# Kernel optimization log

Hardware: AMD Instinct MI355X
Metric: run time of the kernel (lower is better)

Reference implementation:

```python
import jax, jax.numpy as jnp
import numpy as np

D_MODEL = 1024
N_HEADS = 16
D_HEAD = D_MODEL // N_HEADS
SEQ = 2048
BATCH = 2


def setup_inputs() -> dict:
    key = jax.random.key(0)
    ks = jax.random.split(key, 9)
    s = 1.0 / np.sqrt(D_MODEL)
    inp = {
        "x": jax.random.normal(ks[0], (BATCH, SEQ, D_MODEL), dtype=jnp.float32),
        "Wq": jax.random.uniform(ks[1], (D_MODEL, D_MODEL), jnp.float32, -s, s),
        "bq": jax.random.uniform(ks[2], (D_MODEL,), jnp.float32, -s, s),
        "Wk": jax.random.uniform(ks[3], (D_MODEL, D_MODEL), jnp.float32, -s, s),
        "bk": jax.random.uniform(ks[4], (D_MODEL,), jnp.float32, -s, s),
        "Wv": jax.random.uniform(ks[5], (D_MODEL, D_MODEL), jnp.float32, -s, s),
        "bv": jax.random.uniform(ks[6], (D_MODEL,), jnp.float32, -s, s),
        "Wo": jax.random.uniform(ks[7], (D_MODEL, D_MODEL), jnp.float32, -s, s),
        "bo": jax.random.uniform(ks[8], (D_MODEL,), jnp.float32, -s, s),
    }
    return inp


def reference(x, Wq, bq, Wk, bk, Wv, bv, Wo, bo):
    B, S, D = x.shape
    H, Dh = N_HEADS, D_HEAD
    # QKV projections (nn.Linear: x @ W.T + b; here W stored as [in, out])
    q = (x @ Wq + bq).reshape(B, S, H, Dh).transpose(0, 2, 1, 3)  # [B,H,S,Dh]
    k = (x @ Wk + bk).reshape(B, S, H, Dh).transpose(0, 2, 1, 3)
    v = (x @ Wv + bv).reshape(B, S, H, Dh).transpose(0, 2, 1, 3)
    scores = jnp.einsum("bhqd,bhkd->bhqk", q, k) / jnp.sqrt(jnp.float32(Dh))
    causal = jnp.tril(jnp.ones((S, S), dtype=bool))  # [S,S]
    scores = jnp.where(causal[None, None], scores, jnp.float32(-jnp.inf))
    attn = jax.nn.softmax(scores, axis=-1)
    # dropout is identity in eval mode
    h = jnp.einsum("bhqk,bhkd->bhqd", attn, v)  # [B,H,S,Dh]
    h = h.transpose(0, 2, 1, 3).reshape(B, S, D)
    return h @ Wo + bo
```

## Files before the change

### kernel.cpp

```cpp
#include <hip/hip_runtime.h>

typedef unsigned short u16;
typedef unsigned int u32;
typedef __attribute__((ext_vector_type(8))) __bf16 bf16x8;
typedef __attribute__((ext_vector_type(4))) float f32x4;
typedef __attribute__((ext_vector_type(4))) unsigned short u16x4;

#define SEQ 2048
#define DM 1024
#define NH 16
#define DH 64

__device__ __forceinline__ float fexp2(float x) {
  return __builtin_amdgcn_exp2f(x);
}

__device__ __forceinline__ unsigned short f2bf(float f) {
  unsigned u = __builtin_bit_cast(unsigned, f);
  u += 0x7fffu + ((u >> 16) & 1u);
  return (unsigned short)(u >> 16);
}

__device__ __forceinline__ void gload_lds16(const u16* g, u16* l) {
  __builtin_amdgcn_global_load_lds(
      (const __attribute__((address_space(1))) u16*)g,
      (__attribute__((address_space(3))) u16*)l, 16, 0, 0);
}

__global__ __launch_bounds__(256) void cvt_kernel(const float* __restrict__ in,
                                                  u16* __restrict__ out, int n4) {
  int id = blockIdx.x * 256 + threadIdx.x;
  if (id >= n4) return;
  float4 v = ((const float4*)in)[id];
  u16x4 o = { f2bf(v.x), f2bf(v.y), f2bf(v.z), f2bf(v.w) };
  ((u16x4*)out)[id] = o;
}

__global__ __launch_bounds__(256) void wtrans_kernel(const float* __restrict__ W0,
                                                     const float* __restrict__ W1,
                                                     const float* __restrict__ W2,
                                                     const float* __restrict__ W3,
                                                     u16* __restrict__ WtBase) {
  const float* W = (blockIdx.z == 0) ? W0 : (blockIdx.z == 1) ? W1
                 : (blockIdx.z == 2) ? W2 : W3;
  u16* Wt = WtBase + ((size_t)blockIdx.z << 20);
  __shared__ float tile[32][33];
  int tx = threadIdx.x & 31, ty = threadIdx.x >> 5;
  int k0 = blockIdx.y * 32, n0 = blockIdx.x * 32;
#pragma unroll
  for (int j = 0; j < 32; j += 8)
    tile[ty + j][tx] = W[(size_t)(k0 + ty + j) * DM + n0 + tx];
  __syncthreads();
#pragma unroll
  for (int j = 0; j < 32; j += 8)
    Wt[(size_t)(n0 + ty + j) * DM + k0 + tx] = f2bf(tile[tx][ty + j]);
}

__global__ __launch_bounds__(256) void gemm_kernel(
    const u16* __restrict__ A, const u16* __restrict__ WtBase,
    const float* __restrict__ b0, const float* __restrict__ b1,
    const float* __restrict__ b2,
    void* __restrict__ O0, void* __restrict__ O1, void* __restrict__ O2,
    int modeBase) {
  const int Kd = 1024, Nd = 1024;
  const int mode = modeBase + blockIdx.z;
  const u16* Bt = WtBase + (size_t)blockIdx.z * (1u << 20);
  const float* bias = (blockIdx.z == 0) ? b0 : (blockIdx.z == 1) ? b1 : b2;
  void* Out = (blockIdx.z == 0) ? O0 : (blockIdx.z == 1) ? O1 : O2;

  __shared__ u16 As[2][4096];
  __shared__ u16 Bs[2][4096];
  const int tid = threadIdx.x;
  const int lane = tid & 63, w = tid >> 6;
  const int lrow = lane & 15, u = lane >> 4;
  const int wr = w >> 1, wc = w & 1;
  const int brow = blockIdx.y * 128, bcol = blockIdx.x * 128;

  f32x4 acc[4][4] = {};

  const int srow = tid >> 2;
  const int scol = (tid & 3) * 8;
  const u16* a0 = A + (size_t)(brow + srow) * Kd + scol;
  const u16* a1 = A + (size_t)(brow + 64 + srow) * Kd + scol;
  const u16* bt0 = Bt + (size_t)(bcol + srow) * Kd + scol;
  const u16* bt1 = Bt + (size_t)(bcol + 64 + srow) * Kd + scol;

  auto stage = [&](int kt, int buf) {
    gload_lds16(a0 + kt, As[buf] + w * 512);
    gload_lds16(a1 + kt, As[buf] + 2048 + w * 512);
    gload_lds16(bt0 + kt, Bs[buf] + w * 512);
    gload_lds16(bt1 + kt, Bs[buf] + 2048 + w * 512);
  };

  stage(0, 0);
  __syncthreads();

  for (int it = 0; it < 32; ++it) {
    const int cur = it & 1;
    if (it + 1 < 32) stage((it + 1) * 32, cur ^ 1);
    bf16x8 af[4], bfr[4];
#pragma unroll
    for (int m = 0; m < 4; ++m)
      af[m] = *(const bf16x8*)(As[cur] + (wr * 64 + m * 16 + lrow) * 32 + u * 8);
#pragma unroll
    for (int n = 0; n < 4; ++n)
      bfr[n] = *(const bf16x8*)(Bs[cur] + (wc * 64 + n * 16 + lrow) * 32 + u * 8);
#pragma unroll
    for (int m = 0; m < 4; ++m)
#pragma unroll
      for (int n = 0; n < 4; ++n)
        acc[m][n] = __builtin_amdgcn_mfma_f32_16x16x32_bf16(af[m], bfr[n], acc[m][n], 0, 0, 0);
    __syncthreads();
  }

  const int r0 = brow + wr * 64 + u * 4;
  const int c0 = bcol + wc * 64 + lrow;
#pragma unroll
  for (int m = 0; m < 4; ++m) {
#pragma unroll
    for (int n = 0; n < 4; ++n) {
      const int col = c0 + n * 16;
      const float bv = bias[col];
      if (mode == 3) {
        float* O = (float*)Out;
#pragma unroll
        for (int i = 0; i < 4; ++i) {
          int row = r0 + m * 16 + i;
          O[(size_t)row * Nd + col] = acc[m][n][i] + bv;
        }
      } else if (mode == 2) {
        const int rowb = r0 + m * 16;
        const int b = rowb >> 11, s = rowb & 2047;
        const int h = col >> 6, dh = col & 63;
        u16x4 pk;
#pragma unroll
        for (int i = 0; i < 4; ++i) pk[i] = f2bf(acc[m][n][i] + bv);
        u16* O = (u16*)Out;
        *(u16x4*)(O + ((size_t)((b * NH + h) * DH + dh) * SEQ + s)) = pk;
      } else {
        const float sc = (mode == 0) ? 0.1803368801111204f : 1.0f;
        u16* O = (u16*)Out;
#pragma unroll
        for (int i = 0; i < 4; ++i) {
          int row = r0 + m * 16 + i;
          int b = row >> 11, s = row & 2047;
          int h = col >> 6, dh = col & 63;
          O[((size_t)(b * NH + h) * SEQ + s) * DH + dh] = f2bf((acc[m][n][i] + bv) * sc);
        }
      }
    }
  }
}

__device__ __forceinline__ void process_tile(
    const u16* bufK, const u16* bufV, u16* ps,
    const bf16x8 (&qf)[2], f32x4 (&hacc)[4], float& m_i, float& l_i,
    int lrow, int u, int wq, bool diag) {
  f32x4 s[4] = {};
#pragma unroll
  for (int ks = 0; ks < 2; ++ks) {
    const int c = ks * 64 + u * 16;
#pragma unroll
    for (int g = 0; g < 4; ++g) {
      const int r = g * 16 + lrow;
      const bf16x8 kf = *(const bf16x8*)(bufK + ((r * 128 + (c ^ ((r & 7) << 4))) >> 1));
      s[g] = __builtin_amdgcn_mfma_f32_16x16x32_bf16(kf, qf[ks], s[g], 0, 0, 0);
    }
  }
  if (diag) {
#pragma unroll
    for (int g = 0; g < 4; ++g) {
      const int kb = g * 16 + u * 4;
#pragma unroll
      for (int i = 0; i < 4; ++i)
        if (kb + i > wq) s[g][i] = -1e30f;
    }
  }
  float pg[4];
#pragma unroll
  for (int g = 0; g < 4; ++g)
    pg[g] = fmaxf(fmaxf(s[g][0], s[g][1]), fmaxf(s[g][2], s[g][3]));
  float pmax = fmaxf(fmaxf(pg[0], pg[1]), fmaxf(pg[2], pg[3]));
  pmax = fmaxf(pmax, __shfl_xor(pmax, 16));
  pmax = fmaxf(pmax, __shfl_xor(pmax, 32));
  const float mnew = fmaxf(m_i, pmax);
  const float scl = fexp2(m_i - mnew);
  float rs = 0.f;
#pragma unroll
  for (int g = 0; g < 4; ++g)
#pragma unroll
    for (int i = 0; i < 4; ++i) {
      const float p = fexp2(s[g][i] - mnew);
      s[g][i] = p;
      rs += p;
    }
  rs += __shfl_xor(rs, 16);
  rs += __shfl_xor(rs, 32);
  l_i = l_i * scl + rs;
  m_i = mnew;
#pragma unroll
  for (int g = 0; g < 4; ++g) hacc[g] *= scl;
#pragma unroll
  for (int g = 0; g < 4; ++g)
#pragma unroll
    for (int h = 0; h < 2; ++h) {
      const u32 w32 = (u32)f2bf(s[g][2 * h]) | ((u32)f2bf(s[g][2 * h + 1]) << 16);
      const int cb = (g * 16 + u * 4 + 2 * h) * 2;
      *(u32*)(ps + ((lrow * 128 + (cb ^ ((lrow & 7) << 4))) >> 1)) = w32;
    }
#pragma unroll
  for (int ks = 0; ks < 2; ++ks) {
    const int c = ks * 64 + u * 16;
    const bf16x8 pf = *(const bf16x8*)(ps + ((lrow * 128 + (c ^ ((lrow & 7) << 4))) >> 1));
#pragma unroll
    for (int g = 0; g < 4; ++g) {
      const int r = g * 16 + lrow;
      const bf16x8 vf = *(const bf16x8*)(bufV + ((r * 128 + (c ^ ((r & 7) << 4))) >> 1));
      hacc[g] = __builtin_amdgcn_mfma_f32_16x16x32_bf16(vf, pf, hacc[g], 0, 0, 0);
    }
  }
}

__global__ __launch_bounds__(256, 2) void attn_kernel(const u16* __restrict__ Qb,
                                                      const u16* __restrict__ Kb,
                                                      const u16* __restrict__ Vt,
                                                      u16* __restrict__ Hh) {
  const int px = blockIdx.x, bh = blockIdx.y;
  const int qtA = px, qtB = 31 - px;
  const int tid = threadIdx.x, lane = tid & 63, w = tid >> 6;
  const int lrow = lane & 15, u = lane >> 4;

  const u16* Qp = Qb + (size_t)bh * SEQ * DH;
  const u16* Kp = Kb + (size_t)bh * SEQ * DH;
  const u16* Vp = Vt + (size_t)bh * DH * SEQ;

  __shared__ u16 KV[2][2][4096];
  __shared__ u16 Ps[4][1024];

  const int q0A = qtA * 64 + w * 16, q0B = qtB * 64 + w * 16;
  bf16x8 qfA[2], qfB[2];
#pragma unroll
  for (int ks = 0; ks < 2; ++ks) {
    qfA[ks] = *(const bf16x8*)(Qp + (size_t)(q0A + lrow) * DH + ks * 32 + u * 8);
    qfB[ks] = *(const bf16x8*)(Qp + (size_t)(q0B + lrow) * DH + ks * 32 + u * 8);
  }

  float mA = -1e30f, lA = 0.f, mB = -1e30f, lB = 0.f;
  f32x4 haccA[4], haccB[4];
#pragma unroll
  for (int g = 0; g < 4; ++g) {
    haccA[g] = (f32x4){0.f, 0.f, 0.f, 0.f};
    haccB[g] = (f32x4){0.f, 0.f, 0.f, 0.f};
  }

  auto stage = [&](int kt, int buf) {
#pragma unroll
    for (int i = 0; i < 2; ++i) {
      const int p = i * 4096 + tid * 16;
      const int row = p >> 7;
      const int c16 = ((p >> 4) & 7) ^ (row & 7);
      gload_lds16(Kp + (size_t)(kt * 64 + row) * 64 + c16 * 8, &KV[buf][0][p >> 1]);
      gload_lds16(Vp + (size_t)row * 2048 + (size_t)kt * 64 + c16 * 8, &KV[buf][1][p >> 1]);
    }
  };

  stage(0, 0);
  __syncthreads();

  const int wq = w * 16 + lrow;
  const int nkt = qtB + 1;
  for (int kt = 0; kt < nkt; ++kt) {
    const int cur = kt & 1;
    if (kt + 1 < nkt) stage(kt + 1, cur ^ 1);
    if (kt <= qtA)
      process_tile(KV[cur][0], KV[cur][1], Ps[w], qfA, haccA, mA, lA, lrow, u, wq, kt == qtA);
    process_tile(KV[cur][0], KV[cur][1], Ps[w], qfB, haccB, mB, lB, lrow, u, wq, kt == qtB);
    __syncthreads();
  }

  const int b = bh >> 4, h = bh & 15;
  {
    const float inv = 1.0f / lA;
    u16* dst = Hh + ((size_t)b * SEQ + (q0A + lrow)) * DM + h * DH + u * 4;
#pragma unroll
    for (int g = 0; g < 4; ++g) {
      u16x4 pk = { f2bf(haccA[g][0] * inv), f2bf(haccA[g][1] * inv),
                   f2bf(haccA[g][2] * inv), f2bf(haccA[g][3] * inv) };
      *(u16x4*)(dst + g * 16) = pk;
    }
  }
  {
    const float inv = 1.0f / lB;
    u16* dst = Hh + ((size_t)b * SEQ + (q0B + lrow)) * DM + h * DH + u * 4;
#pragma unroll
    for (int g = 0; g < 4; ++g) {
      u16x4 pk = { f2bf(haccB[g][0] * inv), f2bf(haccB[g][1] * inv),
                   f2bf(haccB[g][2] * inv), f2bf(haccB[g][3] * inv) };
      *(u16x4*)(dst + g * 16) = pk;
    }
  }
}

extern "C" void kernel_launch(void* const* d_in, const int* in_sizes, int n_in,
                              void* d_out, int out_size, void* d_ws, size_t ws_size,
                              hipStream_t stream) {
  const float* x  = (const float*)d_in[0];
  const float* Wq = (const float*)d_in[1];
  const float* bq = (const float*)d_in[2];
  const float* Wk = (const float*)d_in[3];
  const float* bk = (const float*)d_in[4];
  const float* Wv = (const float*)d_in[5];
  const float* bv = (const float*)d_in[6];
  const float* Wo = (const float*)d_in[7];
  const float* bo = (const float*)d_in[8];
  float* out = (float*)d_out;

  char* ws = (char*)d_ws;
  u16* Xb  = (u16*)(ws);
  u16* Wt  = (u16*)(ws + (8u << 20));
  u16* Qb  = (u16*)(ws + (16u << 20));
  u16* Kb  = (u16*)(ws + (24u << 20));
  u16* Vt  = (u16*)(ws + (32u << 20));
  u16* Hh  = (u16*)(ws + (40u << 20));
  (void)in_sizes; (void)n_in; (void)out_size; (void)ws_size;

  cvt_kernel<<<4096, 256, 0, stream>>>(x, Xb, 4096 * 1024 / 4);
  dim3 tg(32, 32, 4);
  wtrans_kernel<<<tg, 256, 0, stream>>>(Wq, Wk, Wv, Wo, Wt);
  dim3 gq(8, 32, 3);
  gemm_kernel<<<gq, 256, 0, stream>>>(Xb, Wt, bq, bk, bv, Qb, Kb, Vt, 0);
  dim3 ga(16, 32);
  attn_kernel<<<ga, 256, 0, stream>>>(Qb, Kb, Vt, Hh);
  dim3 go(8, 32, 1);
  gemm_kernel<<<go, 256, 0, stream>>>(Hh, Wt + (3u << 20), bo, bo, bo, out, out, out, 3);
}
```

Before: 204.3 us.

## Interleave dual-query attention tiles, lazy softmax rescale, packed bf16 cvt, smaller GEMM tiles

The attention loop now loads K and V fragments once per tile and shares them between the two query tiles. It also interleaves their MFMAs and gives each query tile its own P scratch buffer. Softmax rescaling is skipped unless the running max grows by more than 8 (in log2 units), which cuts exp work and accumulator scaling but lets unnormalised values reach up to 2^8. Float-to-bf16 conversion uses the hardware packed-convert instruction, and the GEMMs are templated onto smaller tiles to launch more blocks. The extra fragment registers may raise register pressure.

```diff
diff --git a/kernel.cpp b/kernel.cpp
--- a/kernel.cpp
+++ b/kernel.cpp
@@ -5,6 +5,7 @@
 typedef __attribute__((ext_vector_type(8))) __bf16 bf16x8;
 typedef __attribute__((ext_vector_type(4))) float f32x4;
 typedef __attribute__((ext_vector_type(4))) unsigned short u16x4;
+typedef __attribute__((ext_vector_type(2))) unsigned int u32x2;
 
 #define SEQ 2048
 #define DM 1024
@@ -19,6 +20,12 @@
   unsigned u = __builtin_bit_cast(unsigned, f);
   u += 0x7fffu + ((u >> 16) & 1u);
   return (unsigned short)(u >> 16);
+}
+
+__device__ __forceinline__ u32 cvtpk(float lo, float hi) {
+  u32 r;
+  asm("v_cvt_pk_bf16_f32 %0, %1, %2" : "=v"(r) : "v"(lo), "v"(hi));
+  return r;
 }
 
 __device__ __forceinline__ void gload_lds16(const u16* g, u16* l) {
@@ -56,40 +63,42 @@
     Wt[(size_t)(n0 + ty + j) * DM + k0 + tx] = f2bf(tile[tx][ty + j]);
 }
 
+template <int BM, int BN>
 __global__ __launch_bounds__(256) void gemm_kernel(
     const u16* __restrict__ A, const u16* __restrict__ WtBase,
     const float* __restrict__ b0, const float* __restrict__ b1,
     const float* __restrict__ b2,
     void* __restrict__ O0, void* __restrict__ O1, void* __restrict__ O2,
     int modeBase) {
+  constexpr int MR = BM / 32, NR = BN / 32;
   const int Kd = 1024, Nd = 1024;
   const int mode = modeBase + blockIdx.z;
-  const u16* Bt = WtBase + (size_t)blockIdx.z * (1u << 20);
+  const u16* Bt = WtBase + ((size_t)blockIdx.z << 20);
   const float* bias = (blockIdx.z == 0) ? b0 : (blockIdx.z == 1) ? b1 : b2;
   void* Out = (blockIdx.z == 0) ? O0 : (blockIdx.z == 1) ? O1 : O2;
 
-  __shared__ u16 As[2][4096];
-  __shared__ u16 Bs[2][4096];
+  __shared__ u16 As[2][BM * 32];
+  __shared__ u16 Bs[2][BN * 32];
   const int tid = threadIdx.x;
   const int lane = tid & 63, w = tid >> 6;
   const int lrow = lane & 15, u = lane >> 4;
   const int wr = w >> 1, wc = w & 1;
-  const int brow = blockIdx.y * 128, bcol = blockIdx.x * 128;
-
-  f32x4 acc[4][4] = {};
+  const int brow = blockIdx.y * BM, bcol = blockIdx.x * BN;
+
+  f32x4 acc[MR][NR] = {};
 
   const int srow = tid >> 2;
   const int scol = (tid & 3) * 8;
-  const u16* a0 = A + (size_t)(brow + srow) * Kd + scol;
-  const u16* a1 = A + (size_t)(brow + 64 + srow) * Kd + scol;
-  const u16* bt0 = Bt + (size_t)(bcol + srow) * Kd + scol;
-  const u16* bt1 = Bt + (size_t)(bcol + 64 + srow) * Kd + scol;
+  const u16* aP = A + (size_t)(brow + srow) * Kd + scol;
+  const u16* bP = Bt + (size_t)(bcol + srow) * Kd + scol;
 
   auto stage = [&](int kt, int buf) {
-    gload_lds16(a0 + kt, As[buf] + w * 512);
-    gload_lds16(a1 + kt, As[buf] + 2048 + w * 512);
-    gload_lds16(bt0 + kt, Bs[buf] + w * 512);
-    gload_lds16(bt1 + kt, Bs[buf] + 2048 + w * 512);
+#pragma unroll
+    for (int i = 0; i < BM / 64; ++i)
+      gload_lds16(aP + (size_t)i * 64 * Kd + kt, As[buf] + i * 2048 + w * 512);
+#pragma unroll
+    for (int i = 0; i < BN / 64; ++i)
+      gload_lds16(bP + (size_t)i * 64 * Kd + kt, Bs[buf] + i * 2048 + w * 512);
   };
 
   stage(0, 0);
@@ -98,27 +107,27 @@
   for (int it = 0; it < 32; ++it) {
     const int cur = it & 1;
     if (it + 1 < 32) stage((it + 1) * 32, cur ^ 1);
-    bf16x8 af[4], bfr[4];
-#pragma unroll
-    for (int m = 0; m < 4; ++m)
-      af[m] = *(const bf16x8*)(As[cur] + (wr * 64 + m * 16 + lrow) * 32 + u * 8);
-#pragma unroll
-    for (int n = 0; n < 4; ++n)
-      bfr[n] = *(const bf16x8*)(Bs[cur] + (wc * 64 + n * 16 + lrow) * 32 + u * 8);
-#pragma unroll
-    for (int m = 0; m < 4; ++m)
-#pragma unroll
-      for (int n = 0; n < 4; ++n)
+    bf16x8 af[MR], bfr[NR];
+#pragma unroll
+    for (int m = 0; m < MR; ++m)
+      af[m] = *(const bf16x8*)(As[cur] + (wr * (BM / 2) + m * 16 + lrow) * 32 + u * 8);
+#pragma unroll
+    for (int n = 0; n < NR; ++n)
+      bfr[n] = *(const bf16x8*)(Bs[cur] + (wc * (BN / 2) + n * 16 + lrow) * 32 + u * 8);
+#pragma unroll
+    for (int m = 0; m < MR; ++m)
+#pragma unroll
+      for (int n = 0; n < NR; ++n)
         acc[m][n] = __builtin_amdgcn_mfma_f32_16x16x32_bf16(af[m], bfr[n], acc[m][n], 0, 0, 0);
     __syncthreads();
   }
 
-  const int r0 = brow + wr * 64 + u * 4;
-  const int c0 = bcol + wc * 64 + lrow;
-#pragma unroll
-  for (int m = 0; m < 4; ++m) {
-#pragma unroll
-    for (int n = 0; n < 4; ++n) {
+  const int r0 = brow + wr * (BM / 2) + u * 4;
+  const int c0 = bcol + wc * (BN / 2) + lrow;
+#pragma unroll
+  for (int m = 0; m < MR; ++m) {
+#pragma unroll
+    for (int n = 0; n < NR; ++n) {
       const int col = c0 + n * 16;
       const float bv = bias[col];
       if (mode == 3) {
@@ -152,72 +161,42 @@
   }
 }
 
-__device__ __forceinline__ void process_tile(
-    const u16* bufK, const u16* bufV, u16* ps,
-    const bf16x8 (&qf)[2], f32x4 (&hacc)[4], float& m_i, float& l_i,
-    int lrow, int u, int wq, bool diag) {
-  f32x4 s[4] = {};
-#pragma unroll
-  for (int ks = 0; ks < 2; ++ks) {
-    const int c = ks * 64 + u * 16;
-#pragma unroll
-    for (int g = 0; g < 4; ++g) {
-      const int r = g * 16 + lrow;
-      const bf16x8 kf = *(const bf16x8*)(bufK + ((r * 128 + (c ^ ((r & 7) << 4))) >> 1));
-      s[g] = __builtin_amdgcn_mfma_f32_16x16x32_bf16(kf, qf[ks], s[g], 0, 0, 0);
-    }
-  }
-  if (diag) {
-#pragma unroll
-    for (int g = 0; g < 4; ++g) {
-      const int kb = g * 16 + u * 4;
-#pragma unroll
-      for (int i = 0; i < 4; ++i)
-        if (kb + i > wq) s[g][i] = -1e30f;
-    }
-  }
-  float pg[4];
-#pragma unroll
-  for (int g = 0; g < 4; ++g)
-    pg[g] = fmaxf(fmaxf(s[g][0], s[g][1]), fmaxf(s[g][2], s[g][3]));
-  float pmax = fmaxf(fmaxf(pg[0], pg[1]), fmaxf(pg[2], pg[3]));
+__device__ __forceinline__ void softmax_update(f32x4 (&s)[4], f32x4 (&hacc)[4],
+                                               float& m_i, float& l_i) {
+  float pg0 = fmaxf(fmaxf(s[0][0], s[0][1]), fmaxf(s[0][2], s[0][3]));
+  float pg1 = fmaxf(fmaxf(s[1][0], s[1][1]), fmaxf(s[1][2], s[1][3]));
+  float pg2 = fmaxf(fmaxf(s[2][0], s[2][1]), fmaxf(s[2][2], s[2][3]));
+  float pg3 = fmaxf(fmaxf(s[3][0], s[3][1]), fmaxf(s[3][2], s[3][3]));
+  float pmax = fmaxf(fmaxf(pg0, pg1), fmaxf(pg2, pg3));
   pmax = fmaxf(pmax, __shfl_xor(pmax, 16));
   pmax = fmaxf(pmax, __shfl_xor(pmax, 32));
-  const float mnew = fmaxf(m_i, pmax);
-  const float scl = fexp2(m_i - mnew);
+  if (__any(pmax > m_i + 8.0f)) {
+    const float mnew = fmaxf(m_i, pmax);
+    const float scl = fexp2(m_i - mnew);
+    l_i *= scl;
+#pragma unroll
+    for (int g = 0; g < 4; ++g) hacc[g] *= scl;
+    m_i = mnew;
+  }
   float rs = 0.f;
 #pragma unroll
   for (int g = 0; g < 4; ++g)
 #pragma unroll
     for (int i = 0; i < 4; ++i) {
-      const float p = fexp2(s[g][i] - mnew);
+      const float p = fexp2(s[g][i] - m_i);
       s[g][i] = p;
       rs += p;
     }
   rs += __shfl_xor(rs, 16);
   rs += __shfl_xor(rs, 32);
-  l_i = l_i * scl + rs;
-  m_i = mnew;
-#pragma unroll
-  for (int g = 0; g < 4; ++g) hacc[g] *= scl;
-#pragma unroll
-  for (int g = 0; g < 4; ++g)
-#pragma unroll
-    for (int h = 0; h < 2; ++h) {
-      const u32 w32 = (u32)f2bf(s[g][2 * h]) | ((u32)f2bf(s[g][2 * h + 1]) << 16);
-      const int cb = (g * 16 + u * 4 + 2 * h) * 2;
-      *(u32*)(ps + ((lrow * 128 + (cb ^ ((lrow & 7) << 4))) >> 1)) = w32;
-    }
-#pragma unroll
-  for (int ks = 0; ks < 2; ++ks) {
-    const int c = ks * 64 + u * 16;
-    const bf16x8 pf = *(const bf16x8*)(ps + ((lrow * 128 + (c ^ ((lrow & 7) << 4))) >> 1));
-#pragma unroll
-    for (int g = 0; g < 4; ++g) {
-      const int r = g * 16 + lrow;
-      const bf16x8 vf = *(const bf16x8*)(bufV + ((r * 128 + (c ^ ((r & 7) << 4))) >> 1));
-      hacc[g] = __builtin_amdgcn_mfma_f32_16x16x32_bf16(vf, pf, hacc[g], 0, 0, 0);
-    }
+  l_i += rs;
+}
+
+__device__ __forceinline__ void write_p(u16* ps, const f32x4 (&s)[4], int lrow, int u) {
+#pragma unroll
+  for (int g = 0; g < 4; ++g) {
+    u32x2 pw = { cvtpk(s[g][0], s[g][1]), cvtpk(s[g][2], s[g][3]) };
+    *(u32x2*)(ps + ((lrow * 128 + ((g * 32 + u * 8) ^ ((lrow & 7) << 4))) >> 1)) = pw;
   }
 }
 
@@ -235,7 +214,7 @@
   const u16* Vp = Vt + (size_t)bh * DH * SEQ;
 
   __shared__ u16 KV[2][2][4096];
-  __shared__ u16 Ps[4][1024];
+  __shared__ u16 Ps[4][2][1024];
 
   const int q0A = qtA * 64 + w * 16, q0B = qtB * 64 + w * 16;
   bf16x8 qfA[2], qfB[2];
@@ -272,9 +251,82 @@
   for (int kt = 0; kt < nkt; ++kt) {
     const int cur = kt & 1;
     if (kt + 1 < nkt) stage(kt + 1, cur ^ 1);
-    if (kt <= qtA)
-      process_tile(KV[cur][0], KV[cur][1], Ps[w], qfA, haccA, mA, lA, lrow, u, wq, kt == qtA);
-    process_tile(KV[cur][0], KV[cur][1], Ps[w], qfB, haccB, mB, lB, lrow, u, wq, kt == qtB);
+    const u16* bufK = KV[cur][0];
+    const u16* bufV = KV[cur][1];
+    const bool doA = (kt <= qtA);
+
+    bf16x8 kf[2][4];
+#pragma unroll
+    for (int ks = 0; ks < 2; ++ks) {
+      const int c = ks * 64 + u * 16;
+#pragma unroll
+      for (int g = 0; g < 4; ++g) {
+        const int r = g * 16 + lrow;
+        kf[ks][g] = *(const bf16x8*)(bufK + ((r * 128 + (c ^ ((r & 7) << 4))) >> 1));
+      }
+    }
+    f32x4 sA[4] = {}, sB[4] = {};
+#pragma unroll
+    for (int ks = 0; ks < 2; ++ks)
+#pragma unroll
+      for (int g = 0; g < 4; ++g)
+        sB[g] = __builtin_amdgcn_mfma_f32_16x16x32_bf16(kf[ks][g], qfB[ks], sB[g], 0, 0, 0);
+    if (doA) {
+#pragma unroll
+      for (int ks = 0; ks < 2; ++ks)
+#pragma unroll
+        for (int g = 0; g < 4; ++g)
+          sA[g] = __builtin_amdgcn_mfma_f32_16x16x32_bf16(kf[ks][g], qfA[ks], sA[g], 0, 0, 0);
+    }
+    if (kt == qtB) {
+#pragma unroll
+      for (int g = 0; g < 4; ++g) {
+        const int kb = g * 16 + u * 4;
+#pragma unroll
+        for (int i = 0; i < 4; ++i)
+          if (kb + i > wq) sB[g][i] = -1e30f;
+      }
+    }
+    softmax_update(sB, haccB, mB, lB);
+    write_p(&Ps[w][1][0], sB, lrow, u);
+    if (doA) {
+      if (kt == qtA) {
+#pragma unroll
+        for (int g = 0; g < 4; ++g) {
+          const int kb = g * 16 + u * 4;
+#pragma unroll
+          for (int i = 0; i < 4; ++i)
+            if (kb + i > wq) sA[g][i] = -1e30f;
+        }
+      }
+      softmax_update(sA, haccA, mA, lA);
+      write_p(&Ps[w][0][0], sA, lrow, u);
+    }
+    bf16x8 vf[2][4], pfB[2], pfA[2];
+#pragma unroll
+    for (int ks = 0; ks < 2; ++ks) {
+      const int c = ks * 64 + u * 16;
+#pragma unroll
+      for (int g = 0; g < 4; ++g) {
+        const int r = g * 16 + lrow;
+        vf[ks][g] = *(const bf16x8*)(bufV + ((r * 128 + (c ^ ((r & 7) << 4))) >> 1));
+      }
+      pfB[ks] = *(const bf16x8*)(&Ps[w][1][0] + ((lrow * 128 + (c ^ ((lrow & 7) << 4))) >> 1));
+      if (doA)
+        pfA[ks] = *(const bf16x8*)(&Ps[w][0][0] + ((lrow * 128 + (c ^ ((lrow & 7) << 4))) >> 1));
+    }
+#pragma unroll
+    for (int ks = 0; ks < 2; ++ks)
+#pragma unroll
+      for (int g = 0; g < 4; ++g)
+        haccB[g] = __builtin_amdgcn_mfma_f32_16x16x32_bf16(vf[ks][g], pfB[ks], haccB[g], 0, 0, 0);
+    if (doA) {
+#pragma unroll
+      for (int ks = 0; ks < 2; ++ks)
+#pragma unroll
+        for (int g = 0; g < 4; ++g)
+          haccA[g] = __builtin_amdgcn_mfma_f32_16x16x32_bf16(vf[ks][g], pfA[ks], haccA[g], 0, 0, 0);
+    }
     __syncthreads();
   }
 
@@ -284,9 +336,9 @@
     u16* dst = Hh + ((size_t)b * SEQ + (q0A + lrow)) * DM + h * DH + u * 4;
 #pragma unroll
     for (int g = 0; g < 4; ++g) {
-      u16x4 pk = { f2bf(haccA[g][0] * inv), f2bf(haccA[g][1] * inv),
-                   f2bf(haccA[g][2] * inv), f2bf(haccA[g][3] * inv) };
-      *(u16x4*)(dst + g * 16) = pk;
+      u32x2 pk = { cvtpk(haccA[g][0] * inv, haccA[g][1] * inv),
+                   cvtpk(haccA[g][2] * inv, haccA[g][3] * inv) };
+      *(u32x2*)(dst + g * 16) = pk;
     }
   }
   {
@@ -294,9 +346,9 @@
     u16* dst = Hh + ((size_t)b * SEQ + (q0B + lrow)) * DM + h * DH + u * 4;
 #pragma unroll
     for (int g = 0; g < 4; ++g) {
-      u16x4 pk = { f2bf(haccB[g][0] * inv), f2bf(haccB[g][1] * inv),
-                   f2bf(haccB[g][2] * inv), f2bf(haccB[g][3] * inv) };
-      *(u16x4*)(dst + g * 16) = pk;
+      u32x2 pk = { cvtpk(haccB[g][0] * inv, haccB[g][1] * inv),
+                   cvtpk(haccB[g][2] * inv, haccB[g][3] * inv) };
+      *(u32x2*)(dst + g * 16) = pk;
     }
   }
 }
@@ -327,10 +379,10 @@
   cvt_kernel<<<4096, 256, 0, stream>>>(x, Xb, 4096 * 1024 / 4);
   dim3 tg(32, 32, 4);
   wtrans_kernel<<<tg, 256, 0, stream>>>(Wq, Wk, Wv, Wo, Wt);
-  dim3 gq(8, 32, 3);
-  gemm_kernel<<<gq, 256, 0, stream>>>(Xb, Wt, bq, bk, bv, Qb, Kb, Vt, 0);
+  dim3 gq(16, 32, 3);
+  gemm_kernel<128, 64><<<gq, 256, 0, stream>>>(Xb, Wt, bq, bk, bv, Qb, Kb, Vt, 0);
   dim3 ga(16, 32);
   attn_kernel<<<ga, 256, 0, stream>>>(Qb, Kb, Vt, Hh);
-  dim3 go(8, 32, 1);
-  gemm_kernel<<<go, 256, 0, stream>>>(Hh, Wt + (3u << 20), bo, bo, bo, out, out, out, 3);
-}
+  dim3 go(16, 64, 1);
+  gemm_kernel<64, 64><<<go, 256, 0, stream>>>(Hh, Wt + (3u << 20), bo, bo, bo, out, out, out, 3);
+}
```

After: 214.0 us. 1.05x slower.
